# Performance work log

Hardware: AMD Instinct MI355X
Metric: run time of the kernel (lower is better)

Reference implementation:

```python
import jax, jax.numpy as jnp
import numpy as np

N_STATE, N_CTRL, T, NB = 32, 16, 128, 64
NSC = N_STATE + N_CTRL

mT = lambda m: jnp.swapaxes(m, -1, -2)


def setup_inputs() -> dict:
    key = jax.random.key(0)
    k1, k2, k3, k4, k5, k6 = jax.random.split(key, 6)
    # Q must be PSD (the torch example builds Q = Qr^T Qr); add I for conditioning.
    Qr = jax.random.normal(k1, (NB, T, NSC, NSC), jnp.float32)
    Q = mT(Qr) @ Qr / NSC + jnp.eye(NSC, dtype=jnp.float32)
    p = jax.random.normal(k2, (NB, T, NSC), jnp.float32)
    x_init = jax.random.normal(k3, (NB, N_STATE), jnp.float32)
    # Stable-ish linear dynamics so the T=128 rollout does not blow up.
    A = jnp.tile(0.95 * jnp.eye(N_STATE, dtype=jnp.float32), (NB, 1, 1)) \
        + 0.02 * jax.random.normal(k4, (NB, N_STATE, N_STATE), jnp.float32)
    Bm = 0.1 * jax.random.normal(k5, (NB, N_STATE, N_CTRL), jnp.float32)
    c1 = 0.1 * jax.random.normal(k6, (NB, N_STATE), jnp.float32)
    return {"x_init": x_init, "Q": Q, "p": p, "A": A, "Bm": Bm, "c1": c1}


def _gains(Qt, qt, ns):
    # Qt: [B, nsc, nsc], qt: [B, nsc, 1]
    Qxx, Qxu = Qt[:, :ns, :ns], Qt[:, :ns, ns:]
    Qux, Quu = Qt[:, ns:, :ns], Qt[:, ns:, ns:]
    qx, qu = qt[:, :ns], qt[:, ns:]
    Quu_inv = jnp.linalg.pinv(Quu)          # batched pinv, as in the torch code
    K = -(Quu_inv @ Qux)                    # [B, nc, ns]
    k = -(Quu_inv @ qu)                     # [B, nc, 1]
    KT = mT(K)
    V = Qxx + Qxu @ K + KT @ Qux + KT @ Quu @ K
    v = qx + Qxu @ k + KT @ qu + KT @ Quu @ k
    return K, k, V, v


def _lqr(x_init, Q, p, A, Bm, c1):
    ns = A.shape[-1]
    F = jnp.concatenate([A, Bm], axis=-1)   # [B, ns, nsc]
    FT = mT(F)
    ft = c1[..., None]                       # [B, ns, 1]

    # ---- backward Riccati/DP recursion (sequential over T) ----
    K_last, k_last, V, v = _gains(Q[:, -1], p[:, -1][..., None], ns)

    def bstep(carry, inp):
        Vtp1, vtp1 = carry
        Qt_raw, pt = inp                     # [B,nsc,nsc], [B,nsc]
        Qt = Qt_raw + FT @ Vtp1 @ F
        qt = pt[..., None] + FT @ (Vtp1 @ ft) + FT @ vtp1
        K, k, Vt, vt = _gains(Qt, qt, ns)
        return (Vt, vt), (K, k)

    Qtm = jnp.swapaxes(Q[:, :-1], 0, 1)[::-1]   # [T-1, B, nsc, nsc], t = T-2..0
    ptm = jnp.swapaxes(p[:, :-1], 0, 1)[::-1]
    _, (Ks_rev, ks_rev) = jax.lax.scan(bstep, (V, v), (Qtm, ptm))
    Ks = jnp.concatenate([Ks_rev[::-1], K_last[None]], axis=0)  # [T, B, nc, ns], forward time order
    ks = jnp.concatenate([ks_rev[::-1], k_last[None]], axis=0)  # [T, B, nc, 1]

    # ---- forward rollout ----
    def fstep(x, inp):
        K, k, Qt, pt = inp
        u = jnp.einsum('bij,bj->bi', K, x) + k[..., 0]
        xu = jnp.concatenate([x, u], axis=-1)                 # tau_t, [B, nsc]
        obj = 0.5 * jnp.einsum('bi,bij,bj->b', xu, Qt, xu) + jnp.einsum('bi,bi->b', xu, pt)
        xn = jnp.einsum('bij,bj->bi', A, x) + jnp.einsum('bij,bj->bi', Bm, u) + c1
        return xn, (x, u, obj, xu)

    Qf = jnp.swapaxes(Q, 0, 1)               # [T, B, nsc, nsc]
    pf = jnp.swapaxes(p, 0, 1)
    _, (xs, us, objs, taus) = jax.lax.scan(fstep, x_init, (Ks, ks, Qf, pf))
    # xs: [T, B, ns] (x_0..x_{T-1}, matching torch which does not append x_T)
    return xs, us, objs, taus


def reference(x_init, Q, p, A, Bm, c1):
    return _lqr(x_init, Q, p, A, Bm, c1)
```

## Files before the change

kernel.cpp:

```cpp
#include <hip/hip_runtime.h>

#define TT     128
#define NBATCH 64

#define BAR()  asm volatile("s_waitcnt lgkmcnt(0)\n\ts_barrier" ::: "memory")
#define BARV() asm volatile("s_waitcnt vmcnt(0) lgkmcnt(0)\n\ts_barrier" ::: "memory")

__device__ __forceinline__ void gload16(const float* g, float* l) {
    __builtin_amdgcn_global_load_lds(
        (__attribute__((address_space(1))) void*)g,
        (__attribute__((address_space(3))) void*)l, 16, 0, 0);
}

__device__ __forceinline__ float rdlane(float v, int l) {
    return __int_as_float(__builtin_amdgcn_readlane(__float_as_int(v), l));
}

__device__ __forceinline__ void inv4(const float4 pr[4], float IP[4][4]) {
    float a00=pr[0].x, a01=pr[0].y, a10=pr[1].x, a11=pr[1].y;
    float b00=pr[0].z, b01=pr[0].w, b10=pr[1].z, b11=pr[1].w;
    float c00=pr[2].x, c01=pr[2].y, c10=pr[3].x, c11=pr[3].y;
    float d00=pr[2].z, d01=pr[2].w, d10=pr[3].z, d11=pr[3].w;
    float r = 1.0f / (a00*a11 - a01*a10);
    float ia00 =  a11*r, ia01 = -a01*r, ia10 = -a10*r, ia11 = a00*r;
    float t00 = ia00*b00 + ia01*b10, t01 = ia00*b01 + ia01*b11;
    float t10 = ia10*b00 + ia11*b10, t11 = ia10*b01 + ia11*b11;
    float u00 = c00*ia00 + c01*ia10, u01 = c00*ia01 + c01*ia11;
    float u10 = c10*ia00 + c11*ia10, u11 = c10*ia01 + c11*ia11;
    float s00 = d00 - (c00*t00 + c01*t10), s01 = d01 - (c00*t01 + c01*t11);
    float s10 = d10 - (c10*t00 + c11*t10), s11 = d11 - (c10*t01 + c11*t11);
    float rs = 1.0f / (s00*s11 - s01*s10);
    float is00 =  s11*rs, is01 = -s01*rs, is10 = -s10*rs, is11 = s00*rs;
    float su00 = is00*u00 + is01*u10, su01 = is00*u01 + is01*u11;
    float su10 = is10*u00 + is11*u10, su11 = is10*u01 + is11*u11;
    IP[0][0] = ia00 + (t00*su00 + t01*su10);
    IP[0][1] = ia01 + (t00*su01 + t01*su11);
    IP[1][0] = ia10 + (t10*su00 + t11*su10);
    IP[1][1] = ia11 + (t10*su01 + t11*su11);
    IP[0][2] = -(t00*is00 + t01*is10);  IP[0][3] = -(t00*is01 + t01*is11);
    IP[1][2] = -(t10*is00 + t11*is10);  IP[1][3] = -(t10*is01 + t11*is11);
    IP[2][0] = -su00; IP[2][1] = -su01;
    IP[3][0] = -su10; IP[3][1] = -su11;
    IP[2][2] = is00;  IP[2][3] = is01;
    IP[3][2] = is10;  IP[3][3] = is11;
}

__global__ __launch_bounds__(256, 1)
void lqr_backward(const float* __restrict__ Q, const float* __restrict__ p,
                  const float* __restrict__ A, const float* __restrict__ Bm,
                  const float* __restrict__ c1, float* __restrict__ Kws)
{
    const int b   = blockIdx.x;
    const int tid = threadIdx.x;

    __shared__ __align__(16) float Fs[32*52];
    __shared__ __align__(16) float Vs[32*36];
    __shared__ __align__(16) float Ms[32*52];
    __shared__ __align__(16) float Xs[48*52];
    __shared__ __align__(16) float Qtb[2][48*48];
    __shared__ __align__(16) float qtb[2][256];
    __shared__ __align__(16) float KKs[16*36];
    __shared__ float vsv[32], fts[32], wv[32];

    const int ai0 = (tid / 12) * 4, ac0 = (tid % 12) * 4;
    const int br0 = (tid / 12) * 4, bc0 = (tid % 12) * 4;
    const int pi  = tid >> 3;
    const int pg  = tid & 7;
    const int pj0 = pg * 4;

    for (int st = tid; st < 256; st += 256) {
        int k = st >> 3, q = st & 7;
        ((float4*)(Fs + k*52))[q] = ((const float4*)A)[(b*32 + k)*8 + q];
    }
    for (int st = tid; st < 128; st += 256) {
        int k = st >> 2, q = st & 3;
        ((float4*)(Fs + k*52))[8 + q] = ((const float4*)Bm)[(b*32 + k)*4 + q];
    }
    for (int st = tid; st < 288; st += 256) ((float4*)Vs)[st] = make_float4(0,0,0,0);
    if (tid < 32) { vsv[tid] = 0.0f; fts[tid] = c1[b*32 + tid]; }

    {
        const float* Qs0 = Q + (size_t)(b*TT + TT-1) * 2304;
        #pragma unroll
        for (int r = 0; r < 3; ++r) {
            int e = r*256 + tid;
            if (e < 576) gload16(Qs0 + e*4, Qtb[0] + e*4);
        }
        if (tid < 12) gload16(p + (size_t)(b*TT + TT-1)*48 + tid*4, qtb[0] + tid*4);
    }
    BARV();

    for (int t = TT-1; t >= 0; --t) {
        const int cur = (TT-1 - t) & 1;
        float* Qtc = Qtb[cur];
        float* qtc = qtb[cur];
        float* Kbase = Kws + (size_t)(b*TT + t) * 528;

        if (tid < 96) {
            float4 a0 = make_float4(0,0,0,0), a1 = a0, a2 = a0, a3 = a0;
            #pragma unroll
            for (int k = 0; k < 32; ++k) {
                float4 v = *(const float4*)(Vs + k*36 + ai0);
                float4 f = *(const float4*)(Fs + k*52 + ac0);
                a0.x += v.x*f.x; a0.y += v.x*f.y; a0.z += v.x*f.z; a0.w += v.x*f.w;
                a1.x += v.y*f.x; a1.y += v.y*f.y; a1.z += v.y*f.z; a1.w += v.y*f.w;
                a2.x += v.z*f.x; a2.y += v.z*f.y; a2.z += v.z*f.z; a2.w += v.z*f.w;
                a3.x += v.w*f.x; a3.y += v.w*f.y; a3.z += v.w*f.z; a3.w += v.w*f.w;
            }
            *(float4*)(Ms + (ai0+0)*52 + ac0) = a0;
            *(float4*)(Ms + (ai0+1)*52 + ac0) = a1;
            *(float4*)(Ms + (ai0+2)*52 + ac0) = a2;
            *(float4*)(Ms + (ai0+3)*52 + ac0) = a3;
        } else if (tid >= 192) {
            const int idx = tid - 192;
            if (t > 0) {
                const float* Qs = Q + (size_t)(b*TT + t-1) * 2304;
                float* dst = Qtb[cur ^ 1];
                #pragma unroll
                for (int r = 0; r < 9; ++r) {
                    int e = r*64 + idx;
                    gload16(Qs + e*4, dst + e*4);
                }
                if (idx < 12) gload16(p + (size_t)(b*TT + t-1)*48 + idx*4,
                                      qtb[cur ^ 1] + idx*4);
            }
            if (idx < 32) {
                float acc = vsv[idx];
                #pragma unroll
                for (int k = 0; k < 32; ++k) acc += Vs[idx*36 + k] * fts[k];
                wv[idx] = acc;
            }
        }
        BAR();

        if (tid < 144) {
            float4 a0 = *(const float4*)(Qtc + (br0+0)*48 + bc0);
            float4 a1 = *(const float4*)(Qtc + (br0+1)*48 + bc0);
            float4 a2 = *(const float4*)(Qtc + (br0+2)*48 + bc0);
            float4 a3 = *(const float4*)(Qtc + (br0+3)*48 + bc0);
            #pragma unroll
            for (int k = 0; k < 32; ++k) {
                float4 fr = *(const float4*)(Fs + k*52 + br0);
                float4 mc = *(const float4*)(Ms + k*52 + bc0);
                a0.x += fr.x*mc.x; a0.y += fr.x*mc.y; a0.z += fr.x*mc.z; a0.w += fr.x*mc.w;
                a1.x += fr.y*mc.x; a1.y += fr.y*mc.y; a1.z += fr.y*mc.z; a1.w += fr.y*mc.w;
                a2.x += fr.z*mc.x; a2.y += fr.z*mc.y; a2.z += fr.z*mc.z; a2.w += fr.z*mc.w;
                a3.x += fr.w*mc.x; a3.y += fr.w*mc.y; a3.z += fr.w*mc.z; a3.w += fr.w*mc.w;
            }
            *(float4*)(Xs + (br0+0)*52 + bc0) = a0;
            *(float4*)(Xs + (br0+1)*52 + bc0) = a1;
            *(float4*)(Xs + (br0+2)*52 + bc0) = a2;
            *(float4*)(Xs + (br0+3)*52 + bc0) = a3;
        } else if (tid >= 192 && tid < 240) {
            const int c = tid - 192;
            float acc = qtc[c];
            #pragma unroll
            for (int k = 0; k < 32; ++k) acc += Fs[k*52 + c] * wv[k];
            qtc[c] = acc;
            if (c >= 32) Xs[c*52 + 48] = acc;
        }
        BAR();

        float4 pa0; float pq[16];
        if (tid < 64) {
            const int c = (tid < 49) ? tid : 48;
            float col[16];
            #pragma unroll
            for (int r = 0; r < 16; ++r) col[r] = Xs[(32+r)*52 + c];

            #pragma unroll
            for (int q = 0; q < 4; ++q) {
                const int pc = 32 + 4*q;
                float4 pr[4];
                #pragma unroll
                for (int m = 0; m < 4; ++m) {
                    pr[m].x = rdlane(col[4*q+m], pc+0);
                    pr[m].y = rdlane(col[4*q+m], pc+1);
                    pr[m].z = rdlane(col[4*q+m], pc+2);
                    pr[m].w = rdlane(col[4*q+m], pc+3);
                }
                float IP[4][4];
                inv4(pr, IP);
                float R[4];
                #pragma unroll
                for (int m = 0; m < 4; ++m)
                    R[m] = IP[m][0]*col[4*q+0] + IP[m][1]*col[4*q+1]
                         + IP[m][2]*col[4*q+2] + IP[m][3]*col[4*q+3];
                #pragma unroll
                for (int r = 0; r < 16; ++r) {
                    if ((r >> 2) == q) continue;
                    float f0 = rdlane(col[r], pc+0);
                    float f1 = rdlane(col[r], pc+1);
                    float f2 = rdlane(col[r], pc+2);
                    float f3 = rdlane(col[r], pc+3);
                    col[r] -= f0*R[0] + f1*R[1] + f2*R[2] + f3*R[3];
                }
                #pragma unroll
                for (int m = 0; m < 4; ++m) col[4*q+m] = R[m];
            }

            if (tid < 32) {
                #pragma unroll
                for (int r = 0; r < 16; ++r) {
                    KKs[r*36 + c]    = col[r];
                    Kbase[c*16 + r]  = -col[r];
                }
            } else if (tid == 48) {
                #pragma unroll
                for (int r = 0; r < 16; ++r) {
                    KKs[r*36 + 32]   = col[r];
                    Kbase[512 + r]   = -col[r];
                }
            }
        } else {
            pa0 = *(const float4*)(Xs + pi*52 + pj0);
            #pragma unroll
            for (int m = 0; m < 4; ++m) {
                float4 v4 = *(const float4*)(Xs + pi*52 + 32 + m*4);
                pq[m*4+0] = v4.x; pq[m*4+1] = v4.y;
                pq[m*4+2] = v4.z; pq[m*4+3] = v4.w;
            }
        }
        BAR();

        {
            if (tid < 64) {
                pa0 = *(const float4*)(Xs + pi*52 + pj0);
                #pragma unroll
                for (int m = 0; m < 4; ++m) {
                    float4 v4 = *(const float4*)(Xs + pi*52 + 32 + m*4);
                    pq[m*4+0] = v4.x; pq[m*4+1] = v4.y;
                    pq[m*4+2] = v4.z; pq[m*4+3] = v4.w;
                }
            }
            #pragma unroll
            for (int k = 0; k < 16; ++k) {
                float4 k0 = *(const float4*)(KKs + k*36 + pj0);
                pa0.x -= pq[k]*k0.x; pa0.y -= pq[k]*k0.y;
                pa0.z -= pq[k]*k0.z; pa0.w -= pq[k]*k0.w;
            }
            *(float4*)(Vs + pi*36 + pj0) = pa0;
            if (pg == 0) {
                float accv = qtc[pi];
                #pragma unroll
                for (int k = 0; k < 16; ++k) accv -= pq[k] * KKs[k*36 + 32];
                vsv[pi] = accv;
            }
        }
        BARV();
    }
}

__global__ __launch_bounds__(64, 1)
void lqr_forward(const float* __restrict__ Kws, const float* __restrict__ A,
                 const float* __restrict__ Bm, const float* __restrict__ c1,
                 const float* __restrict__ x_init,
                 float* __restrict__ xs, float* __restrict__ us,
                 float* __restrict__ taus)
{
    const int b = blockIdx.x, l = threadIdx.x;
    __shared__ __align__(16) float Fb[32*48];
    __shared__ __align__(16) float Kb[544];
    __shared__ float c1s[32], xu[48];

    for (int st = l; st < 256; st += 64) {
        int k = st >> 3, q = st & 7;
        ((float4*)Fb)[k*12 + q] = ((const float4*)A)[(b*32 + k)*8 + q];
    }
    for (int st = l; st < 128; st += 64) {
        int k = st >> 2, q = st & 3;
        ((float4*)Fb)[k*12 + 8 + q] = ((const float4*)Bm)[(b*32 + k)*4 + q];
    }
    if (l < 32) { c1s[l] = c1[b*32 + l]; xu[l] = x_init[b*32 + l]; }

    float4 ka, kb, kc = make_float4(0,0,0,0);
    {
        const float4* s0 = (const float4*)(Kws + (size_t)(b*TT) * 528);
        ka = s0[l]; kb = s0[l + 64];
        if (l < 4) kc = s0[l + 128];
    }
    __syncthreads();

    for (int t = 0; t < TT; ++t) {
        ((float4*)Kb)[l]      = ka;
        ((float4*)Kb)[l + 64] = kb;
        if (l < 4) ((float4*)Kb)[l + 128] = kc;
        __syncthreads();

        if (t + 1 < TT) {
            const float4* sn = (const float4*)(Kws + (size_t)(b*TT + t+1) * 528);
            ka = sn[l]; kb = sn[l + 64];
            if (l < 4) kc = sn[l + 128];
        }

        float part = 0.0f;
        int i = l & 15, g = l >> 4;
        #pragma unroll
        for (int jj = 0; jj < 8; ++jj) {
            int j = g*8 + jj;
            part += Kb[j*16 + i] * xu[j];
        }
        part += __shfl_down(part, 32);
        part += __shfl_down(part, 16);
        float ui = part + Kb[512 + i];
        if (l < 16) {
            xu[32 + l] = ui;
            us[(size_t)(t*64 + b)*16 + l] = ui;
        }
        __syncthreads();

        if (l < 32) xs[(size_t)(t*64 + b)*32 + l] = xu[l];
        if (l < 48) taus[(size_t)(t*64 + b)*48 + l] = xu[l];

        float pn = 0.0f;
        int i2 = l & 31, h = l >> 5;
        #pragma unroll
        for (int jj = 0; jj < 24; ++jj) {
            int j = h*24 + jj;
            pn += Fb[i2*48 + j] * xu[j];
        }
        pn += __shfl_down(pn, 32);
        float xni = pn + ((l < 32) ? c1s[i2] : 0.0f);
        __syncthreads();
        if (l < 32) xu[l] = xni;
        __syncthreads();
    }
}

__global__ __launch_bounds__(256, 4)
void lqr_obj(const float* __restrict__ Q, const float* __restrict__ p,
             const float* __restrict__ taus, float* __restrict__ objs)
{
    const int bi = blockIdx.x;
    const int b = bi >> 7, t = bi & 127;
    const int tid = threadIdx.x;
    __shared__ float xu[48];
    __shared__ float red[8];
    const float* tp = taus + (size_t)(t*64 + b)*48;
    if (tid < 48) xu[tid] = tp[tid];
    __syncthreads();

    const float4* Q4 = (const float4*)(Q + (size_t)bi * 2304);
    float acc = 0.0f;
    for (int e4 = tid; e4 < 576; e4 += 256) {
        float4 qv = Q4[e4];
        int r = e4 / 12, c = (e4 % 12) * 4;
        float xr = xu[r];
        acc += xr * (qv.x*xu[c] + qv.y*xu[c+1] + qv.z*xu[c+2] + qv.w*xu[c+3]);
    }
    acc *= 0.5f;
    if (tid < 48) acc += xu[tid] * p[(size_t)bi*48 + tid];

    #pragma unroll
    for (int off = 32; off > 0; off >>= 1) acc += __shfl_down(acc, off);
    if ((tid & 63) == 0) red[tid >> 6] = acc;
    __syncthreads();
    if (tid == 0) objs[(t << 6) + b] = red[0] + red[1] + red[2] + red[3];
}

extern "C" void kernel_launch(void* const* d_in, const int* in_sizes, int n_in,
                              void* d_out, int out_size, void* d_ws, size_t ws_size,
                              hipStream_t stream) {
    const float* x_init = (const float*)d_in[0];
    const float* Q      = (const float*)d_in[1];
    const float* p      = (const float*)d_in[2];
    const float* A      = (const float*)d_in[3];
    const float* Bm     = (const float*)d_in[4];
    const float* c1     = (const float*)d_in[5];

    float* out  = (float*)d_out;
    float* xs   = out;
    float* us   = out + 262144;
    float* objs = out + 393216;
    float* taus = out + 401408;

    float* Kws = (float*)d_ws;

    lqr_backward<<<NBATCH, 256, 0, stream>>>(Q, p, A, Bm, c1, Kws);
    lqr_forward<<<NBATCH, 64, 0, stream>>>(Kws, A, Bm, c1, x_init, xs, us, taus);
    lqr_obj<<<NBATCH*TT, 256, 0, stream>>>(Q, p, taus, objs);
}
```

Before: 684.9 us.

## Replicate Quu block solve in every wave to drop a barrier and KKs staging

All four waves now run the redundant 16x16 block-elimination solve on their own lanes, so each wave holds the K columns in registers. This removes the shared KKs staging buffer and one block-wide barrier per time step. The V update is then computed straight from registers: each wave handles 8 rows and the upper lanes of wave 3 compute v. The final vmcnt(0) barrier is replaced by a partial s_waitcnt vmcnt(10) in the prefetching wave, which lets global-to-LDS prefetches stay in flight across iterations. In exchange every wave repeats the inversion arithmetic, and the wait count has to match the number of outstanding loads exactly.

```diff
diff --git a/kernel.cpp b/kernel.cpp
--- a/kernel.cpp
+++ b/kernel.cpp
@@ -52,6 +52,8 @@
 {
     const int b   = blockIdx.x;
     const int tid = threadIdx.x;
+    const int lane = tid & 63;
+    const int wv8  = tid >> 6;
 
     __shared__ __align__(16) float Fs[32*52];
     __shared__ __align__(16) float Vs[32*36];
@@ -59,14 +61,10 @@
     __shared__ __align__(16) float Xs[48*52];
     __shared__ __align__(16) float Qtb[2][48*48];
     __shared__ __align__(16) float qtb[2][256];
-    __shared__ __align__(16) float KKs[16*36];
-    __shared__ float vsv[32], fts[32], wv[32];
+    __shared__ float vsv[32], fts[32], wvv[32];
 
     const int ai0 = (tid / 12) * 4, ac0 = (tid % 12) * 4;
     const int br0 = (tid / 12) * 4, bc0 = (tid % 12) * 4;
-    const int pi  = tid >> 3;
-    const int pg  = tid & 7;
-    const int pj0 = pg * 4;
 
     for (int st = tid; st < 256; st += 256) {
         int k = st >> 3, q = st & 7;
@@ -128,8 +126,12 @@
                 float acc = vsv[idx];
                 #pragma unroll
                 for (int k = 0; k < 32; ++k) acc += Vs[idx*36 + k] * fts[k];
-                wv[idx] = acc;
-            }
+                wvv[idx] = acc;
+            }
+        }
+        if (tid >= 192) {
+            if (t > 0) asm volatile("s_waitcnt vmcnt(10)" ::: "memory");
+            else       asm volatile("s_waitcnt vmcnt(0)"  ::: "memory");
         }
         BAR();
 
@@ -155,15 +157,14 @@
             const int c = tid - 192;
             float acc = qtc[c];
             #pragma unroll
-            for (int k = 0; k < 32; ++k) acc += Fs[k*52 + c] * wv[k];
+            for (int k = 0; k < 32; ++k) acc += Fs[k*52 + c] * wvv[k];
             qtc[c] = acc;
             if (c >= 32) Xs[c*52 + 48] = acc;
         }
         BAR();
 
-        float4 pa0; float pq[16];
-        if (tid < 64) {
-            const int c = (tid < 49) ? tid : 48;
+        {
+            const int c = (lane < 49) ? lane : 48;
             float col[16];
             #pragma unroll
             for (int r = 0; r < 16; ++r) col[r] = Xs[(32+r)*52 + c];
@@ -200,54 +201,48 @@
             }
 
             if (tid < 32) {
-                #pragma unroll
-                for (int r = 0; r < 16; ++r) {
-                    KKs[r*36 + c]    = col[r];
-                    Kbase[c*16 + r]  = -col[r];
+                float* kb = Kbase + tid*16;
+                *(float4*)(kb+ 0) = make_float4(-col[0],-col[1],-col[2],-col[3]);
+                *(float4*)(kb+ 4) = make_float4(-col[4],-col[5],-col[6],-col[7]);
+                *(float4*)(kb+ 8) = make_float4(-col[8],-col[9],-col[10],-col[11]);
+                *(float4*)(kb+12) = make_float4(-col[12],-col[13],-col[14],-col[15]);
+            } else if (tid == 48) {
+                float* kb = Kbase + 512;
+                *(float4*)(kb+ 0) = make_float4(-col[0],-col[1],-col[2],-col[3]);
+                *(float4*)(kb+ 4) = make_float4(-col[4],-col[5],-col[6],-col[7]);
+                *(float4*)(kb+ 8) = make_float4(-col[8],-col[9],-col[10],-col[11]);
+                *(float4*)(kb+12) = make_float4(-col[12],-col[13],-col[14],-col[15]);
+            }
+
+            if (lane < 32) {
+                const int j = lane;
+                #pragma unroll
+                for (int ii = 0; ii < 8; ++ii) {
+                    const int i = wv8*8 + ii;
+                    float4 q0 = *(const float4*)(Xs + i*52 + 32);
+                    float4 q1 = *(const float4*)(Xs + i*52 + 36);
+                    float4 q2 = *(const float4*)(Xs + i*52 + 40);
+                    float4 q3 = *(const float4*)(Xs + i*52 + 44);
+                    float acc = Xs[i*52 + j];
+                    acc -= q0.x*col[0]  + q0.y*col[1]  + q0.z*col[2]  + q0.w*col[3];
+                    acc -= q1.x*col[4]  + q1.y*col[5]  + q1.z*col[6]  + q1.w*col[7];
+                    acc -= q2.x*col[8]  + q2.y*col[9]  + q2.z*col[10] + q2.w*col[11];
+                    acc -= q3.x*col[12] + q3.y*col[13] + q3.z*col[14] + q3.w*col[15];
+                    Vs[i*36 + j] = acc;
                 }
-            } else if (tid == 48) {
-                #pragma unroll
-                for (int r = 0; r < 16; ++r) {
-                    KKs[r*36 + 32]   = col[r];
-                    Kbase[512 + r]   = -col[r];
-                }
-            }
-        } else {
-            pa0 = *(const float4*)(Xs + pi*52 + pj0);
-            #pragma unroll
-            for (int m = 0; m < 4; ++m) {
-                float4 v4 = *(const float4*)(Xs + pi*52 + 32 + m*4);
-                pq[m*4+0] = v4.x; pq[m*4+1] = v4.y;
-                pq[m*4+2] = v4.z; pq[m*4+3] = v4.w;
+            } else if (tid >= 224) {
+                const int i = tid - 224;
+                float kkr[16];
+                #pragma unroll
+                for (int r = 0; r < 16; ++r) kkr[r] = rdlane(col[r], 48);
+                float accv = qtc[i];
+                #pragma unroll
+                for (int k = 0; k < 16; ++k)
+                    accv -= Xs[i*52 + 32 + k] * kkr[k];
+                vsv[i] = accv;
             }
         }
         BAR();
-
-        {
-            if (tid < 64) {
-                pa0 = *(const float4*)(Xs + pi*52 + pj0);
-                #pragma unroll
-                for (int m = 0; m < 4; ++m) {
-                    float4 v4 = *(const float4*)(Xs + pi*52 + 32 + m*4);
-                    pq[m*4+0] = v4.x; pq[m*4+1] = v4.y;
-                    pq[m*4+2] = v4.z; pq[m*4+3] = v4.w;
-                }
-            }
-            #pragma unroll
-            for (int k = 0; k < 16; ++k) {
-                float4 k0 = *(const float4*)(KKs + k*36 + pj0);
-                pa0.x -= pq[k]*k0.x; pa0.y -= pq[k]*k0.y;
-                pa0.z -= pq[k]*k0.z; pa0.w -= pq[k]*k0.w;
-            }
-            *(float4*)(Vs + pi*36 + pj0) = pa0;
-            if (pg == 0) {
-                float accv = qtc[pi];
-                #pragma unroll
-                for (int k = 0; k < 16; ++k) accv -= pq[k] * KKs[k*36 + 32];
-                vsv[pi] = accv;
-            }
-        }
-        BARV();
     }
 }
 
```

Result: slower. 715.6 us (+4.5%).
